# Performance work log

Measured on AMD Instinct MI355X. Metric: run time of the kernel, lower is better.

## Reference

```python
import jax, jax.numpy as jnp
import numpy as np


def setup_inputs() -> dict:
    key = jax.random.key(0)
    ks = jax.random.split(key, 6)
    shapes = [
        (2048, 128, 64),   # large: shape[1] > 64
        (2048, 32, 32),    # small -> fused bucket
        (2048, 64, 64),    # small (== 64 is not > 64) -> fused bucket
        (2048, 16, 48),    # small -> fused bucket
        (2048, 200, 32),   # large: shape[1] > 64
        (2048, 8, 8),      # small -> fused bucket
    ]
    inp = {f"x{i}": jax.random.normal(ks[i], s, dtype=jnp.float32) for i, s in enumerate(shapes)}
    inp["dim"] = 1  # dim[0] in the original module: reduce over the middle (list-length) axis
    return inp


def reference(x0, x1, x2, x3, x4, x5, dim):
    # ComboSumModule: outputs[i] = input_list[i].sum(dim[0]).
    # The size-bucketing (shape[1]>64 or shape[2]>64) only changes kernel
    # fusion, not the math, so each tensor is reduced independently.
    xs = (x0, x1, x2, x3, x4, x5)
    return tuple(jnp.sum(x, axis=dim) for x in xs)
```

## Files before the change

### kernel.cpp

```cpp
#include <hip/hip_runtime.h>


template <int M, int N>
__device__ __forceinline__ void col_sum(const float* __restrict__ xp,
                                        float* __restrict__ out,
                                        int local, int out_base4) {
  constexpr int N4 = N / 4;
  static_assert(M % 4 == 0, "M divisible by 4");
  const int b  = local / N4;
  const int n4 = local - b * N4;
  const float4* __restrict__ p =
      reinterpret_cast<const float4*>(xp) + (size_t)b * (M * N4) + n4;

  float4 a0 = make_float4(0.f, 0.f, 0.f, 0.f);
  float4 a1 = make_float4(0.f, 0.f, 0.f, 0.f);
  float4 a2 = make_float4(0.f, 0.f, 0.f, 0.f);
  float4 a3 = make_float4(0.f, 0.f, 0.f, 0.f);

#pragma unroll 2
  for (int m = 0; m < M; m += 4) {
    float4 v0 = p[(size_t)(m + 0) * N4];
    float4 v1 = p[(size_t)(m + 1) * N4];
    float4 v2 = p[(size_t)(m + 2) * N4];
    float4 v3 = p[(size_t)(m + 3) * N4];
    a0.x += v0.x; a0.y += v0.y; a0.z += v0.z; a0.w += v0.w;
    a1.x += v1.x; a1.y += v1.y; a1.z += v1.z; a1.w += v1.w;
    a2.x += v2.x; a2.y += v2.y; a2.z += v2.z; a2.w += v2.w;
    a3.x += v3.x; a3.y += v3.y; a3.z += v3.z; a3.w += v3.w;
  }

  float4 r;
  r.x = (a0.x + a1.x) + (a2.x + a3.x);
  r.y = (a0.y + a1.y) + (a2.y + a3.y);
  r.z = (a0.z + a1.z) + (a2.z + a3.z);
  r.w = (a0.w + a1.w) + (a2.w + a3.w);
  reinterpret_cast<float4*>(out)[out_base4 + local] = r;
}

__global__ __launch_bounds__(64) void ComboSumModule_25314537242674_kernel(
    const float* __restrict__ x0, const float* __restrict__ x1,
    const float* __restrict__ x2, const float* __restrict__ x3,
    const float* __restrict__ x4, const float* __restrict__ x5,
    float* __restrict__ out) {
  const int u = blockIdx.x * 64 + threadIdx.x;
  if (u < 32768) {
    col_sum<128, 64>(x0, out, u, 0);
  } else if (u < 49152) {
    col_sum<32, 32>(x1, out, u - 32768, 32768);
  } else if (u < 81920) {
    col_sum<64, 64>(x2, out, u - 49152, 49152);
  } else if (u < 106496) {
    col_sum<16, 48>(x3, out, u - 81920, 81920);
  } else if (u < 122880) {
    col_sum<200, 32>(x4, out, u - 106496, 106496);
  } else {
    col_sum<8, 8>(x5, out, u - 122880, 122880);
  }
}

extern "C" void kernel_launch(void* const* d_in, const int* in_sizes, int n_in,
                              void* d_out, int out_size, void* d_ws, size_t ws_size,
                              hipStream_t stream) {
  const float* x0 = (const float*)d_in[0];
  const float* x1 = (const float*)d_in[1];
  const float* x2 = (const float*)d_in[2];
  const float* x3 = (const float*)d_in[3];
  const float* x4 = (const float*)d_in[4];
  const float* x5 = (const float*)d_in[5];
  float* out = (float*)d_out;

  ComboSumModule_25314537242674_kernel<<<1984, 64, 0, stream>>>(
      x0, x1, x2, x3, x4, x5, out);
}
```

Before: 181.6 us.

## Split column reductions across four waves per block with LDS combine

Each 64-column group now uses a 256-thread block instead of a 64-thread block. The four waves each sum a quarter of the reduced axis, and wave 0 adds the four partial float4 sums through shared memory. The goal is four times as many memory requests in flight, to hide global-load latency in what looks like a latency-bound reduction. The cost is a block-wide barrier, a small LDS round-trip, and a different floating-point summation order.

```diff
diff --git a/kernel.cpp b/kernel.cpp
--- a/kernel.cpp
+++ b/kernel.cpp
@@ -1,60 +1,63 @@
 #include <hip/hip_runtime.h>
 
+
+__device__ __forceinline__ float4 f4add(float4 a, float4 b) {
+  return make_float4(a.x + b.x, a.y + b.y, a.z + b.z, a.w + b.w);
+}
 
 template <int M, int N>
 __device__ __forceinline__ void col_sum(const float* __restrict__ xp,
                                         float* __restrict__ out,
-                                        int local, int out_base4) {
+                                        int local, int wave, int lane,
+                                        int out_base4, float4* lds) {
   constexpr int N4 = N / 4;
-  static_assert(M % 4 == 0, "M divisible by 4");
+  constexpr int R = M / 4;
+  static_assert(R % 2 == 0, "R divisible by 2");
   const int b  = local / N4;
   const int n4 = local - b * N4;
   const float4* __restrict__ p =
-      reinterpret_cast<const float4*>(xp) + (size_t)b * (M * N4) + n4;
+      reinterpret_cast<const float4*>(xp) + (size_t)b * (M * N4) +
+      (size_t)(wave * R) * N4 + n4;
 
   float4 a0 = make_float4(0.f, 0.f, 0.f, 0.f);
   float4 a1 = make_float4(0.f, 0.f, 0.f, 0.f);
-  float4 a2 = make_float4(0.f, 0.f, 0.f, 0.f);
-  float4 a3 = make_float4(0.f, 0.f, 0.f, 0.f);
-
 #pragma unroll 2
-  for (int m = 0; m < M; m += 4) {
+  for (int m = 0; m < R; m += 2) {
     float4 v0 = p[(size_t)(m + 0) * N4];
     float4 v1 = p[(size_t)(m + 1) * N4];
-    float4 v2 = p[(size_t)(m + 2) * N4];
-    float4 v3 = p[(size_t)(m + 3) * N4];
-    a0.x += v0.x; a0.y += v0.y; a0.z += v0.z; a0.w += v0.w;
-    a1.x += v1.x; a1.y += v1.y; a1.z += v1.z; a1.w += v1.w;
-    a2.x += v2.x; a2.y += v2.y; a2.z += v2.z; a2.w += v2.w;
-    a3.x += v3.x; a3.y += v3.y; a3.z += v3.z; a3.w += v3.w;
+    a0 = f4add(a0, v0);
+    a1 = f4add(a1, v1);
   }
-
-  float4 r;
-  r.x = (a0.x + a1.x) + (a2.x + a3.x);
-  r.y = (a0.y + a1.y) + (a2.y + a3.y);
-  r.z = (a0.z + a1.z) + (a2.z + a3.z);
-  r.w = (a0.w + a1.w) + (a2.w + a3.w);
-  reinterpret_cast<float4*>(out)[out_base4 + local] = r;
+  lds[wave * 64 + lane] = f4add(a0, a1);
+  __syncthreads();
+  if (wave == 0) {
+    float4 r = f4add(f4add(lds[lane], lds[64 + lane]),
+                     f4add(lds[128 + lane], lds[192 + lane]));
+    reinterpret_cast<float4*>(out)[out_base4 + local] = r;
+  }
 }
 
-__global__ __launch_bounds__(64) void ComboSumModule_25314537242674_kernel(
+__global__ __launch_bounds__(256) void ComboSumModule_25314537242674_kernel(
     const float* __restrict__ x0, const float* __restrict__ x1,
     const float* __restrict__ x2, const float* __restrict__ x3,
     const float* __restrict__ x4, const float* __restrict__ x5,
     float* __restrict__ out) {
-  const int u = blockIdx.x * 64 + threadIdx.x;
+  __shared__ float4 lds[4 * 64];
+  const int lane = threadIdx.x & 63;
+  const int wave = threadIdx.x >> 6;
+  const int u = blockIdx.x * 64 + lane;
   if (u < 32768) {
-    col_sum<128, 64>(x0, out, u, 0);
+    col_sum<128, 64>(x0, out, u, wave, lane, 0, lds);
   } else if (u < 49152) {
-    col_sum<32, 32>(x1, out, u - 32768, 32768);
+    col_sum<32, 32>(x1, out, u - 32768, wave, lane, 32768, lds);
   } else if (u < 81920) {
-    col_sum<64, 64>(x2, out, u - 49152, 49152);
+    col_sum<64, 64>(x2, out, u - 49152, wave, lane, 49152, lds);
   } else if (u < 106496) {
-    col_sum<16, 48>(x3, out, u - 81920, 81920);
+    col_sum<16, 48>(x3, out, u - 81920, wave, lane, 81920, lds);
   } else if (u < 122880) {
-    col_sum<200, 32>(x4, out, u - 106496, 106496);
+    col_sum<200, 32>(x4, out, u - 106496, wave, lane, 106496, lds);
   } else {
-    col_sum<8, 8>(x5, out, u - 122880, 122880);
+    col_sum<8, 8>(x5, out, u - 122880, wave, lane, 122880, lds);
   }
 }
 
@@ -69,6 +72,6 @@
   const float* x5 = (const float*)d_in[5];
   float* out = (float*)d_out;
 
-  ComboSumModule_25314537242674_kernel<<<1984, 64, 0, stream>>>(
+  ComboSumModule_25314537242674_kernel<<<1984, 256, 0, stream>>>(
       x0, x1, x2, x3, x4, x5, out);
 }
```

Result: no change. 182.6 us (+0.6%).
